# Kernel tuning notes

Hardware: AMD Instinct MI355X
Metric: run time of the kernel (lower is better)

The kernel has to match this reference:

```python
import jax, jax.numpy as jnp
import numpy as np

N = 4096
HID = 256
H = 4
D = HID // H  # 64
EDGE_DIM = 16
DEG = 32
E = N * DEG
EPS = 1e-5


def _layer_norm(x, g, b):
    m = jnp.mean(x, axis=-1, keepdims=True)
    v = jnp.mean((x - m) ** 2, axis=-1, keepdims=True)
    return (x - m) * jax.lax.rsqrt(v + EPS) * g + b


def setup_inputs() -> dict:
    key = jax.random.key(0)
    ks = jax.random.split(key, 16)
    s = 1.0 / np.sqrt(HID)
    x = jax.random.normal(ks[0], (N, HID), dtype=jnp.float32)
    # ring graph: every node is a src with DEG distinct neighbors -> no empty
    # softmax rows, no duplicate (src, dst) pairs
    src = jnp.repeat(jnp.arange(N, dtype=jnp.int64), DEG)
    dst = (src + jnp.tile(jnp.arange(1, DEG + 1, dtype=jnp.int64), N)) % N
    edge_index = jnp.stack([src, dst], axis=0)
    edge_attr = jax.random.normal(ks[1], (E, EDGE_DIM), dtype=jnp.float32)
    inp = {
        "x": x,
        "edge_index": edge_index,
        "edge_attr": edge_attr,
        "Wq": jax.random.uniform(ks[2], (HID, HID), jnp.float32, -s, s),
        "bq": jnp.zeros((HID,), jnp.float32),
        "Wk": jax.random.uniform(ks[3], (HID, HID), jnp.float32, -s, s),
        "bk": jnp.zeros((HID,), jnp.float32),
        "Wv": jax.random.uniform(ks[4], (HID, HID), jnp.float32, -s, s),
        "bv": jnp.zeros((HID,), jnp.float32),
        "Wo": jax.random.uniform(ks[5], (HID, HID), jnp.float32, -s, s),
        "bo": jnp.zeros((HID,), jnp.float32),
        "We": jax.random.uniform(ks[6], (EDGE_DIM, H), jnp.float32, -1.0 / np.sqrt(EDGE_DIM), 1.0 / np.sqrt(EDGE_DIM)),
        "be": jnp.zeros((H,), jnp.float32),
        "g1": jnp.ones((HID,), jnp.float32),
        "b1": jnp.zeros((HID,), jnp.float32),
        "g2": jnp.ones((HID,), jnp.float32),
        "b2": jnp.zeros((HID,), jnp.float32),
        "Wf1": jax.random.uniform(ks[7], (HID, 4 * HID), jnp.float32, -s, s),
        "bf1": jnp.zeros((4 * HID,), jnp.float32),
        "Wf2": jax.random.uniform(ks[8], (4 * HID, HID), jnp.float32, -1.0 / np.sqrt(4 * HID), 1.0 / np.sqrt(4 * HID)),
        "bf2": jnp.zeros((HID,), jnp.float32),
    }
    return inp


def reference(x, edge_index, edge_attr, Wq, bq, Wk, bk, Wv, bv, Wo, bo,
              We, be, g1, b1, g2, b2, Wf1, bf1, Wf2, bf2):
    src, dst = edge_index[0], edge_index[1]
    q = (x @ Wq + bq).reshape(N, H, D)
    k = (x @ Wk + bk).reshape(N, H, D)
    v = (x @ Wv + bv).reshape(N, H, D)
    edge_bias = edge_attr @ We + be                       # [E, H]
    dot = jnp.sum(q[src] * k[dst], axis=-1) / np.sqrt(D)  # [E, H]
    total_bias = dot + edge_bias                          # [E, H]
    # dense (H, N, N) logits, -inf everywhere except the E edges (as in the
    # original module)
    logits = jnp.full((H, N, N), -jnp.inf, dtype=x.dtype)
    logits = logits.at[:, src, dst].set(total_bias.T)
    attn = jax.nn.softmax(logits, axis=-1)                # [H, N, N]
    out = jnp.einsum('hnm,mhd->nhd', attn, v).reshape(N, HID)
    out = out @ Wo + bo
    x = _layer_norm(x + out, g1, b1)
    ffn = jax.nn.relu(x @ Wf1 + bf1) @ Wf2 + bf2
    x = _layer_norm(x + ffn, g2, b2)
    return x
```

## Files before the change

kernel.cpp:

```cpp
#include <hip/hip_runtime.h>
#include <cstddef>

#define N_NODES 4096
#define HIDDEN  256
#define NHEAD   4
#define DHEAD   64
#define EDGE_DIM 16
#define DEG     32
#define NEDGE   (N_NODES * DEG)
#define LN_EPS  1e-5f
#define QKV_STRIDE 768
#define KV_WIN  47

typedef short  s16x8 __attribute__((ext_vector_type(8)));
typedef float  f32x4 __attribute__((ext_vector_type(4)));
typedef unsigned short u16x8 __attribute__((ext_vector_type(8)));
typedef unsigned short u16x4 __attribute__((ext_vector_type(4)));

__device__ __forceinline__ unsigned short f2b(float f) {
    union { float f; unsigned u; } c{f};
    unsigned u = c.u;
    return (unsigned short)((u + 0x7fffu + ((u >> 16) & 1u)) >> 16);
}
__device__ __forceinline__ float b2f(unsigned short s) {
    union { unsigned u; float f; } c;
    c.u = ((unsigned)s) << 16;
    return c.f;
}
__device__ __forceinline__ int xcd_swz(int bid, int total) {
    const int q = total >> 3;
    return (bid & 7) * q + (bid >> 3);
}

__device__ __forceinline__ void pack_tile(const float* __restrict__ src,
                                          unsigned short* __restrict__ dst,
                                          int K, int Nn, int tt, int rowoff,
                                          float (*tile)[65], int tid) {
    const int tk = K / 64;
    const int k0 = (tt % tk) * 64, n0 = (tt / tk) * 64;

    const int kk = tid >> 2, nq = (tid & 3) * 16;
#pragma unroll
    for (int i = 0; i < 16; i += 4) {
        float4 vv = *(const float4*)&src[(size_t)(k0 + kk) * Nn + n0 + nq + i];
        tile[kk][nq + i + 0] = vv.x;
        tile[kk][nq + i + 1] = vv.y;
        tile[kk][nq + i + 2] = vv.z;
        tile[kk][nq + i + 3] = vv.w;
    }
    __syncthreads();
    const int nn = tid >> 2, kq = (tid & 3) * 16;
    unsigned short tmp[16];
#pragma unroll
    for (int i = 0; i < 16; ++i) tmp[i] = f2b(tile[kq + i][nn]);
    unsigned short* drow = dst + (size_t)(rowoff + n0 + nn) * K + k0 + kq;
    *(u16x8*)(drow + 0) = *(u16x8*)&tmp[0];
    *(u16x8*)(drow + 8) = *(u16x8*)&tmp[8];
}

__global__ __launch_bounds__(256) void pack_kernel(
    const float* __restrict__ Wq, const float* __restrict__ Wk,
    const float* __restrict__ Wv, const float* __restrict__ Wo,
    const float* __restrict__ Wf1, const float* __restrict__ Wf2,
    const float* __restrict__ bq, const float* __restrict__ bk,
    const float* __restrict__ bv,
    unsigned short* __restrict__ Wqkv_t, unsigned short* __restrict__ Wo_t,
    unsigned short* __restrict__ Wf1_t, unsigned short* __restrict__ Wf2_t,
    float* __restrict__ bias768) {
    const int b = blockIdx.x;
    const int tid = threadIdx.x;
    __shared__ float tile[64][65];

    if (b < 48) {
        int m = b / 16, tt = b % 16;
        const float* src = (m == 0) ? Wq : ((m == 1) ? Wk : Wv);
        pack_tile(src, Wqkv_t, 256, 256, tt, m * 256, tile, tid);
    } else if (b < 64) {
        pack_tile(Wo, Wo_t, 256, 256, b - 48, 0, tile, tid);
    } else if (b < 128) {
        pack_tile(Wf1, Wf1_t, 256, 1024, b - 64, 0, tile, tid);
    } else if (b < 192) {
        pack_tile(Wf2, Wf2_t, 1024, 256, b - 128, 0, tile, tid);
    } else {
        bias768[tid]       = bq[tid];
        bias768[256 + tid] = bk[tid];
        bias768[512 + tid] = bv[tid];
    }
}

__global__ __launch_bounds__(256) void gemm_qkv(const float* __restrict__ X,
                                                const unsigned short* __restrict__ Bt,
                                                const float* __restrict__ bias,
                                                unsigned short* __restrict__ Cout) {
    __shared__ unsigned short sA[64 * 64];
    __shared__ unsigned short sB[64 * 64];
    const int tid = threadIdx.x;
    const int wave = tid >> 6, lane = tid & 63;
    const int b2 = xcd_swz(blockIdx.x, 768);
    const int row0 = (b2 / 12) * 64, col0 = (b2 % 12) * 64;
    const int wr = wave >> 1, wc = wave & 1;

    f32x4 acc[2][2] = {};

    const int lo0 = tid * 16, lo1 = lo0 + 4096;
    const int r0 = lo0 >> 7, c0 = lo0 & 127;
    const int r1 = lo1 >> 7, c1 = lo1 & 127;
    const int so0 = (lo0 & ~127) | (c0 ^ ((r0 & 7) << 4));
    const int so1 = (lo1 & ~127) | (c1 ^ ((r1 & 7) << 4));

    const int ar  = tid >> 2;
    const int akb = (tid & 3) * 16;
    const int acb = akb * 2;
    const int axr = (ar & 7) << 4;
    const int aso0 = (ar * 128) | ((acb +  0) ^ axr);
    const int aso1 = (ar * 128) | ((acb + 16) ^ axr);

    float4 f0, f1, f2v, f3;
    s16x8 b0r, b1r;

#define QKV_LOAD(KT)                                                          \
    {                                                                         \
        const float* Ap = X + (size_t)(row0 + ar) * 256 + (KT) * 64 + akb;    \
        f0  = *(const float4*)(Ap + 0);                                       \
        f1  = *(const float4*)(Ap + 4);                                       \
        f2v = *(const float4*)(Ap + 8);                                       \
        f3  = *(const float4*)(Ap + 12);                                      \
        const char* Bb = (const char*)Bt + ((size_t)col0 * 256 + (KT) * 64) * 2; \
        b0r = *(const s16x8*)(Bb + (size_t)r0 * 512 + c0);                    \
        b1r = *(const s16x8*)(Bb + (size_t)r1 * 512 + c1);                    \
    }

    QKV_LOAD(0);
#pragma unroll
    for (int kt = 0; kt < 4; ++kt) {
        if (kt) __syncthreads();
        u16x8 pa0 = {f2b(f0.x), f2b(f0.y), f2b(f0.z), f2b(f0.w),
                     f2b(f1.x), f2b(f1.y), f2b(f1.z), f2b(f1.w)};
        u16x8 pa1 = {f2b(f2v.x), f2b(f2v.y), f2b(f2v.z), f2b(f2v.w),
                     f2b(f3.x), f2b(f3.y), f2b(f3.z), f2b(f3.w)};
        *(u16x8*)((char*)sA + aso0) = pa0;
        *(u16x8*)((char*)sA + aso1) = pa1;
        *(s16x8*)((char*)sB + so0) = b0r;
        *(s16x8*)((char*)sB + so1) = b1r;
        __syncthreads();
        if (kt < 3) QKV_LOAD(kt + 1);

        const char* sAc = (const char*)sA;
        const char* sBc = (const char*)sB;
#pragma unroll
        for (int kk = 0; kk < 64; kk += 32) {
            const int koffb = (kk + ((lane >> 4) << 3)) * 2;
            s16x8 a[2], bfr[2];
#pragma unroll
            for (int m = 0; m < 2; ++m) {
                const int r = wr * 32 + m * 16 + (lane & 15);
                int off = r * 128 + koffb;
                off ^= (r & 7) << 4;
                a[m] = *(const s16x8*)(sAc + off);
            }
#pragma unroll
            for (int n = 0; n < 2; ++n) {
                const int c = wc * 32 + n * 16 + (lane & 15);
                int off = c * 128 + koffb;
                off ^= (c & 7) << 4;
                bfr[n] = *(const s16x8*)(sBc + off);
            }
#pragma unroll
            for (int m = 0; m < 2; ++m)
#pragma unroll
                for (int n = 0; n < 2; ++n)
                    acc[m][n] = __builtin_amdgcn_mfma_f32_16x16x32_bf16(
                        a[m], bfr[n], acc[m][n], 0, 0, 0);
        }
    }
#undef QKV_LOAD

    const int crow = row0 + wr * 32 + ((lane >> 4) << 2);
    const int ccol = col0 + wc * 32 + (lane & 15);
#pragma unroll
    for (int n = 0; n < 2; ++n) {
        const int c = ccol + n * 16;
        const float bv = bias[c];
#pragma unroll
        for (int m = 0; m < 2; ++m)
#pragma unroll
            for (int j = 0; j < 4; ++j)
                Cout[(size_t)(crow + m * 16 + j) * QKV_STRIDE + c] =
                    f2b(acc[m][n][j] + bv);
    }
}

__global__ __launch_bounds__(256) void gemm_ffn1(const unsigned short* __restrict__ A,
                                                 const unsigned short* __restrict__ Bt,
                                                 const float* __restrict__ bias,
                                                 unsigned short* __restrict__ Cout) {
    constexpr int K = 256;
    __shared__ unsigned short sA[64 * 64];
    __shared__ unsigned short sB[128 * 64];
    const int tid = threadIdx.x;
    const int wave = tid >> 6, lane = tid & 63;
    const int b2 = xcd_swz(blockIdx.x, 512);
    const int row0 = (b2 >> 3) * 64, col0 = (b2 & 7) * 128;
    const int wr = wave >> 1, wc = wave & 1;

    f32x4 acc[2][4] = {};

    const int lo0 = tid * 16, lo1 = lo0 + 4096;
    const int r0 = lo0 >> 7, c0 = lo0 & 127;
    const int r1 = lo1 >> 7, c1 = lo1 & 127;
    const int so0 = (lo0 & ~127) | (c0 ^ ((r0 & 7) << 4));
    const int so1 = (lo1 & ~127) | (c1 ^ ((r1 & 7) << 4));

    s16x8 a0r, a1r, breg[4];

#define F1_LOAD(KT)                                                           \
    {                                                                         \
        const char* Ab = (const char*)A + ((size_t)row0 * K + (KT) * 64) * 2; \
        a0r = *(const s16x8*)(Ab + (size_t)r0 * (K * 2) + c0);                \
        a1r = *(const s16x8*)(Ab + (size_t)r1 * (K * 2) + c1);                \
        const char* Bb = (const char*)Bt + ((size_t)col0 * K + (KT) * 64) * 2;\
        _Pragma("unroll")                                                     \
        for (int p = 0; p < 4; ++p) {                                         \
            const int lo = tid * 16 + p * 4096;                               \
            const int r = lo >> 7, c = lo & 127;                              \
            breg[p] = *(const s16x8*)(Bb + (size_t)r * (K * 2) + c);          \
        }                                                                     \
    }

    F1_LOAD(0);
#pragma unroll
    for (int kt = 0; kt < 4; ++kt) {
        if (kt) __syncthreads();
        *(s16x8*)((char*)sA + so0) = a0r;
        *(s16x8*)((char*)sA + so1) = a1r;
#pragma unroll
        for (int p = 0; p < 4; ++p) {
            const int lo = tid * 16 + p * 4096;
            const int r = lo >> 7, c = lo & 127;
            const int so = (lo & ~127) | (c ^ ((r & 7) << 4));
            *(s16x8*)((char*)sB + so) = breg[p];
        }
        __syncthreads();
        if (kt + 1 < 4) F1_LOAD(kt + 1);

        const char* sAc = (const char*)sA;
        const char* sBc = (const char*)sB;
#pragma unroll
        for (int kk = 0; kk < 64; kk += 32) {
            const int koffb = (kk + ((lane >> 4) << 3)) * 2;
            s16x8 a[2], bfr[4];
#pragma unroll
            for (int m = 0; m < 2; ++m) {
                const int r = wr * 32 + m * 16 + (lane & 15);
                int off = r * 128 + koffb;
                off ^= (r & 7) << 4;
                a[m] = *(const s16x8*)(sAc + off);
            }
#pragma unroll
            for (int n = 0; n < 4; ++n) {
                const int c = wc * 64 + n * 16 + (lane & 15);
                int off = c * 128 + koffb;
                off ^= (c & 7) << 4;
                bfr[n] = *(const s16x8*)(sBc + off);
            }
#pragma unroll
            for (int m = 0; m < 2; ++m)
#pragma unroll
                for (int n = 0; n < 4; ++n)
                    acc[m][n] = __builtin_amdgcn_mfma_f32_16x16x32_bf16(
                        a[m], bfr[n], acc[m][n], 0, 0, 0);
        }
    }
#undef F1_LOAD

    const int crow = row0 + wr * 32 + ((lane >> 4) << 2);
    const int ccol = col0 + wc * 64 + (lane & 15);
#pragma unroll
    for (int n = 0; n < 4; ++n) {
        const int c = ccol + n * 16;
        const float bv = bias[c];
#pragma unroll
        for (int m = 0; m < 2; ++m)
#pragma unroll
            for (int j = 0; j < 4; ++j) {
                const int r = crow + m * 16 + j;
                Cout[(size_t)r * 1024 + c] = f2b(fmaxf(acc[m][n][j] + bv, 0.f));
            }
    }
}

__global__ __launch_bounds__(256) void gemm_partial(const unsigned short* __restrict__ A,
                                                    const unsigned short* __restrict__ Bt,
                                                    float* __restrict__ part) {
    constexpr int KF = 1024;
    __shared__ unsigned short sA[64 * 64];
    __shared__ unsigned short sB[64 * 64];
    const int tid = threadIdx.x;
    const int wave = tid >> 6, lane = tid & 63;
    const int b2 = xcd_swz(blockIdx.x, 512);
    const int z = b2 >> 8;
    const int rem = b2 & 255;
    const int row0 = (rem >> 2) * 64, col0 = (rem & 3) * 64;
    const int wr = wave >> 1, wc = wave & 1;

    f32x4 acc[2][2] = {};

    const int lo0 = tid * 16;
    const int lo1 = lo0 + 4096;
    const int r0 = lo0 >> 7, c0 = lo0 & 127;
    const int r1 = lo1 >> 7, c1 = lo1 & 127;
    const int so0 = (lo0 & ~127) | (c0 ^ ((r0 & 7) << 4));
    const int so1 = (lo1 & ~127) | (c1 ^ ((r1 & 7) << 4));

    const char* Abase = (const char*)A + ((size_t)row0 * KF + z * 512) * 2;
    const char* Bbase = (const char*)Bt + ((size_t)col0 * KF + z * 512) * 2;

    s16x8 a0r, a1r, b0r, b1r;

#define GP_LOAD(KT)                                                           \
    {                                                                         \
        a0r = *(const s16x8*)(Abase + (KT) * 128 + (size_t)r0 * (KF * 2) + c0); \
        a1r = *(const s16x8*)(Abase + (KT) * 128 + (size_t)r1 * (KF * 2) + c1); \
        b0r = *(const s16x8*)(Bbase + (KT) * 128 + (size_t)r0 * (KF * 2) + c0); \
        b1r = *(const s16x8*)(Bbase + (KT) * 128 + (size_t)r1 * (KF * 2) + c1); \
    }

    GP_LOAD(0);
#pragma unroll
    for (int kt = 0; kt < 8; ++kt) {
        if (kt) __syncthreads();
        *(s16x8*)((char*)sA + so0) = a0r;
        *(s16x8*)((char*)sA + so1) = a1r;
        *(s16x8*)((char*)sB + so0) = b0r;
        *(s16x8*)((char*)sB + so1) = b1r;
        __syncthreads();
        if (kt + 1 < 8) GP_LOAD(kt + 1);

        const char* sAc = (const char*)sA;
        const char* sBc = (const char*)sB;
#pragma unroll
        for (int kk = 0; kk < 64; kk += 32) {
            const int koffb = (kk + ((lane >> 4) << 3)) * 2;
            s16x8 a[2], bfr[2];
#pragma unroll
            for (int m = 0; m < 2; ++m) {
                const int r = wr * 32 + m * 16 + (lane & 15);
                int off = r * 128 + koffb;
                off ^= (r & 7) << 4;
                a[m] = *(const s16x8*)(sAc + off);
            }
#pragma unroll
            for (int n = 0; n < 2; ++n) {
                const int c = wc * 32 + n * 16 + (lane & 15);
                int off = c * 128 + koffb;
                off ^= (c & 7) << 4;
                bfr[n] = *(const s16x8*)(sBc + off);
            }
#pragma unroll
            for (int m = 0; m < 2; ++m)
#pragma unroll
                for (int n = 0; n < 2; ++n)
                    acc[m][n] = __builtin_amdgcn_mfma_f32_16x16x32_bf16(
                        a[m], bfr[n], acc[m][n], 0, 0, 0);
        }
    }
#undef GP_LOAD

    const int crow = row0 + wr * 32 + ((lane >> 4) << 2);
    const int ccol = col0 + wc * 32 + (lane & 15);
    float* pz = part + (size_t)z * N_NODES * HIDDEN;
#pragma unroll
    for (int n = 0; n < 2; ++n) {
        const int c = ccol + n * 16;
#pragma unroll
        for (int m = 0; m < 2; ++m)
#pragma unroll
            for (int j = 0; j < 4; ++j)
                pz[(size_t)(crow + m * 16 + j) * HIDDEN + c] = acc[m][n][j];
    }
}

__global__ __launch_bounds__(256) void ln2_reduce(const float* __restrict__ part,
                                                  const float* __restrict__ y,
                                                  const float* __restrict__ bf2,
                                                  const float* __restrict__ g2,
                                                  const float* __restrict__ b2,
                                                  float* __restrict__ out) {
    const int tid = threadIdx.x;
    const int row = blockIdx.x * 8 + (tid >> 5);
    const int cb = (tid & 31) * 8;
    const size_t rb = (size_t)row * HIDDEN;
    constexpr size_t ZS = (size_t)N_NODES * HIDDEN;

    float vals[8];
#pragma unroll
    for (int q = 0; q < 2; ++q) {
        const int c = cb + q * 4;
        float4 vy = *(const float4*)&y[rb + c];
        float4 vb = *(const float4*)&bf2[c];
        float4 s0 = *(const float4*)&part[0 * ZS + rb + c];
        float4 s1 = *(const float4*)&part[1 * ZS + rb + c];
        vals[q * 4 + 0] = vy.x + vb.x + s0.x + s1.x;
        vals[q * 4 + 1] = vy.y + vb.y + s0.y + s1.y;
        vals[q * 4 + 2] = vy.z + vb.z + s0.z + s1.z;
        vals[q * 4 + 3] = vy.w + vb.w + s0.w + s1.w;
    }
    float sm = 0.f, sq = 0.f;
#pragma unroll
    for (int i = 0; i < 8; ++i) { sm += vals[i]; sq = fmaf(vals[i], vals[i], sq); }
#pragma unroll
    for (int off = 16; off >= 1; off >>= 1) {
        sm += __shfl_xor(sm, off);
        sq += __shfl_xor(sq, off);
    }
    const float mean = sm * (1.f / HIDDEN);
    const float var  = sq * (1.f / HIDDEN) - mean * mean;
    const float inv  = rsqrtf(var + LN_EPS);
#pragma unroll
    for (int q = 0; q < 2; ++q) {
        const int c = cb + q * 4;
        float4 vg = *(const float4*)&g2[c];
        float4 vbb = *(const float4*)&b2[c];
        float4 o;
        o.x = (vals[q * 4 + 0] - mean) * inv * vg.x + vbb.x;
        o.y = (vals[q * 4 + 1] - mean) * inv * vg.y + vbb.y;
        o.z = (vals[q * 4 + 2] - mean) * inv * vg.z + vbb.z;
        o.w = (vals[q * 4 + 3] - mean) * inv * vg.w + vbb.w;
        *(float4*)&out[rb + c] = o;
    }
}

__global__ __launch_bounds__(512) void attn_oproj_ln(
    const unsigned short* __restrict__ qkv,
    const int* __restrict__ edge_dst,
    const float* __restrict__ edge_attr,
    const float* __restrict__ We, const float* __restrict__ be,
    const unsigned short* __restrict__ Wo_t,
    const float* __restrict__ bo,
    const float* __restrict__ x,
    const float* __restrict__ g, const float* __restrict__ b,
    float* __restrict__ y, unsigned short* __restrict__ yb) {
    __shared__ float sQ[16][260];
    __shared__ float sP[16][NHEAD][DEG];
    __shared__ int   sDst[16][DEG];
    __shared__ float sWe[EDGE_DIM * NHEAD];
    __shared__ unsigned short sKV[2][KV_WIN * 256];
    __shared__ unsigned short sA[16 * 256];
    __shared__ unsigned short sB[2][256 * 64];
    __shared__ float rs[16][8], rq[16][8];

    const int tid = threadIdx.x;
    const int wave = tid >> 6, lane = tid & 63;
    const int n0 = blockIdx.x * 16;

    {
        const int r = tid >> 5, e = (tid & 31) * 8;
        u16x8 v = *(const u16x8*)(qkv + (size_t)(n0 + r) * QKV_STRIDE + e);
#pragma unroll
        for (int i = 0; i < 8; ++i) sQ[r][e + i] = b2f(v[i]);
    }
    for (int t = tid; t < 2 * KV_WIN * 32; t += 512) {
        const int half = (t >= KV_WIN * 32) ? 1 : 0;
        const int tt = t - half * (KV_WIN * 32);
        const int rr = tt >> 5, c16 = tt & 31;
        const int gsrc = (n0 + 1 + rr) & (N_NODES - 1);
        u16x8 v = *(const u16x8*)(qkv + (size_t)gsrc * QKV_STRIDE +
                                  (half ? 512 : 256) + c16 * 8);
        const int so = rr * 512 + ((c16 ^ (rr & 7)) * 16);
        *(u16x8*)((char*)sKV[half] + so) = v;
    }
    if (tid < EDGE_DIM * NHEAD) sWe[tid] = We[tid];
    __syncthreads();

    {
        const int node = tid >> 5, j = tid & 31;
        const int dstj = edge_dst[(n0 + node) * DEG + j];
        sDst[node][j] = dstj;
        const int idx = (dstj - n0 - 1) & (N_NODES - 1);
        const char* krow = (const char*)sKV[0] + idx * 512;
        const int swz = (idx & 7);
        float lg[4];
#pragma unroll
        for (int h = 0; h < 4; ++h) {
            float dot = 0.f;
            const float* qh = &sQ[node][h * 64];
#pragma unroll
            for (int q8 = 0; q8 < 8; ++q8) {
                const int c16 = h * 8 + q8;
                u16x8 kv = *(const u16x8*)(krow + ((c16 ^ swz) * 16));
#pragma unroll
                for (int d = 0; d < 8; ++d)
                    dot = fmaf(qh[q8 * 8 + d], b2f(kv[d]), dot);
            }
            lg[h] = dot * 0.125f + be[h];
        }
        const float* ea_ = edge_attr + (size_t)((n0 + node) * DEG + j) * EDGE_DIM;
#pragma unroll
        for (int c = 0; c < EDGE_DIM; ++c) {
            const float eav = ea_[c];
#pragma unroll
            for (int h = 0; h < 4; ++h)
                lg[h] = fmaf(eav, sWe[c * NHEAD + h], lg[h]);
        }
#pragma unroll
        for (int h = 0; h < 4; ++h) {
            float mx = lg[h];
#pragma unroll
            for (int off = 16; off >= 1; off >>= 1)
                mx = fmaxf(mx, __shfl_xor(mx, off));
            float p = __expf(lg[h] - mx);
            float sum = p;
#pragma unroll
            for (int off = 16; off >= 1; off >>= 1)
                sum += __shfl_xor(sum, off);
            sP[node][h][j] = p / sum;
        }
    }
    __syncthreads();

    {
        const int node = tid >> 5, oct = tid & 31;
        const int h = oct >> 3;
        const int chunk = oct;
        float acc8[8] = {};
#pragma unroll 8
        for (int j = 0; j < DEG; ++j) {
            const float p = sP[node][h][j];
            const int idx = (sDst[node][j] - n0 - 1) & (N_NODES - 1);
            u16x8 vv = *(const u16x8*)((const char*)sKV[1] + idx * 512 +
                                       ((chunk ^ (idx & 7)) * 16));
#pragma unroll
            for (int i = 0; i < 8; ++i) acc8[i] = fmaf(p, b2f(vv[i]), acc8[i]);
        }
        u16x8 pk;
#pragma unroll
        for (int i = 0; i < 8; ++i) pk[i] = f2b(acc8[i]);
        const int so = node * 512 + ((oct * 16) ^ ((node & 7) << 4));
        *(u16x8*)((char*)sA + so) = pk;
    }

    s16x8 breg[4];
#define WO_LOAD(KT)                                                           \
    {                                                                         \
        _Pragma("unroll")                                                     \
        for (int p = 0; p < 4; ++p) {                                         \
            const int lo = tid * 16 + p * 8192;                               \
            const int r = lo >> 7, c = lo & 127;                              \
            breg[p] = *(const s16x8*)((const char*)Wo_t + (size_t)r * 512 +   \
                                      (KT) * 128 + c);                        \
        }                                                                     \
    }
#define WO_STORE(BUF)                                                         \
    {                                                                         \
        _Pragma("unroll")                                                     \
        for (int p = 0; p < 4; ++p) {                                         \
            const int lo = tid * 16 + p * 8192;                               \
            const int r = lo >> 7, c = lo & 127;                              \
            const int so = (lo & ~127) | (c ^ ((r & 7) << 4));                \
            *(s16x8*)((char*)sB[BUF] + so) = breg[p];                         \
        }                                                                     \
    }

    WO_LOAD(0);
    WO_STORE(0);
    __syncthreads();

    f32x4 acc[2] = {};
#pragma unroll
    for (int kt = 0; kt < 4; ++kt) {
        if (kt + 1 < 4) WO_LOAD(kt + 1);

        const char* sBc = (const char*)sB[kt & 1];
#pragma unroll
        for (int kk = 0; kk < 64; kk += 32) {
            const int lk = ((lane >> 4) << 3);
            s16x8 a;
            {
                const int r = lane & 15;
                const int koffb = (kt * 64 + kk + lk) * 2;
                a = *(const s16x8*)((const char*)sA + r * 512 +
                                    (koffb ^ ((r & 7) << 4)));
            }
            s16x8 bfr[2];
            const int boffb = (kk + lk) * 2;
#pragma unroll
            for (int n = 0; n < 2; ++n) {
                const int c = wave * 32 + n * 16 + (lane & 15);
                bfr[n] = *(const s16x8*)(sBc + c * 128 + (boffb ^ ((c & 7) << 4)));
            }
#pragma unroll
            for (int n = 0; n < 2; ++n)
                acc[n] = __builtin_amdgcn_mfma_f32_16x16x32_bf16(a, bfr[n], acc[n], 0, 0, 0);
        }

        if (kt + 1 < 4) {
            WO_STORE((kt + 1) & 1);
            __syncthreads();
        }
    }
#undef WO_LOAD
#undef WO_STORE

    const int rbase = ((lane >> 4) << 2);
    const int cbase = wave * 32 + (lane & 15);

    float sm[4] = {}, sq_[4] = {};
#pragma unroll
    for (int n = 0; n < 2; ++n) {
        const int c = cbase + n * 16;
        const float bv = bo[c];
#pragma unroll
        for (int j = 0; j < 4; ++j) {
            const int r = rbase + j;
            float v = acc[n][j] + bv + x[(size_t)(n0 + r) * HIDDEN + c];
            acc[n][j] = v;
            sm[j] += v;
            sq_[j] = fmaf(v, v, sq_[j]);
        }
    }
#pragma unroll
    for (int off = 8; off >= 1; off >>= 1) {
#pragma unroll
        for (int j = 0; j < 4; ++j) {
            sm[j] += __shfl_xor(sm[j], off);
            sq_[j] += __shfl_xor(sq_[j], off);
        }
    }
    if ((lane & 15) == 0) {
#pragma unroll
        for (int j = 0; j < 4; ++j) {
            rs[rbase + j][wave] = sm[j];
            rq[rbase + j][wave] = sq_[j];
        }
    }
    __syncthreads();

#pragma unroll
    for (int j = 0; j < 4; ++j) {
        const int r = rbase + j;
        float tot = 0.f, totq = 0.f;
#pragma unroll
        for (int w = 0; w < 8; ++w) { tot += rs[r][w]; totq += rq[r][w]; }
        const float mean = tot * (1.f / HIDDEN);
        const float var  = totq * (1.f / HIDDEN) - mean * mean;
        const float inv  = rsqrtf(var + LN_EPS);
#pragma unroll
        for (int n = 0; n < 2; ++n) {
            const int c = cbase + n * 16;
            const float res = (acc[n][j] - mean) * inv * g[c] + b[c];
            y[(size_t)(n0 + r) * HIDDEN + c] = res;
            yb[(size_t)(n0 + r) * HIDDEN + c] = f2b(res);
        }
    }
}

extern "C" void kernel_launch(void* const* d_in, const int* in_sizes, int n_in,
                              void* d_out, int out_size, void* d_ws, size_t ws_size,
                              hipStream_t stream) {
    const float* x   = (const float*)d_in[0];
    const int*   ei  = (const int*)d_in[1];
    const float* ea  = (const float*)d_in[2];
    const float* Wq  = (const float*)d_in[3];
    const float* bq  = (const float*)d_in[4];
    const float* Wk  = (const float*)d_in[5];
    const float* bk  = (const float*)d_in[6];
    const float* Wv  = (const float*)d_in[7];
    const float* bv  = (const float*)d_in[8];
    const float* Wo  = (const float*)d_in[9];
    const float* bo  = (const float*)d_in[10];
    const float* We  = (const float*)d_in[11];
    const float* be  = (const float*)d_in[12];
    const float* g1  = (const float*)d_in[13];
    const float* b1  = (const float*)d_in[14];
    const float* g2  = (const float*)d_in[15];
    const float* b2  = (const float*)d_in[16];
    const float* Wf1 = (const float*)d_in[17];
    const float* bf1 = (const float*)d_in[18];
    const float* Wf2 = (const float*)d_in[19];
    const float* bf2 = (const float*)d_in[20];

    char* W = (char*)d_ws;
    unsigned short* Wqkv_t  = (unsigned short*)(W + (2u << 20));
    unsigned short* Wo_t    = (unsigned short*)(W + (2u << 20) + 384 * 1024);
    unsigned short* Wf1_t   = (unsigned short*)(W + (2u << 20) + 512 * 1024);
    unsigned short* Wf2_t   = (unsigned short*)(W + (2u << 20) + 1024 * 1024);
    float*          bias768 = (float*)(W + (2u << 20) + 1536 * 1024);
    unsigned short* qkvb    = (unsigned short*)(W + (4u << 20));
    unsigned short* h1b     = (unsigned short*)(W + (4u << 20));
    float*          y       = (float*)(W + (12u << 20));
    unsigned short* yb      = (unsigned short*)(W + (16u << 20));
    float*          part    = (float*)(W + (20u << 20));

    const dim3 blk(256);

    pack_kernel<<<193, blk, 0, stream>>>(Wq, Wk, Wv, Wo, Wf1, Wf2, bq, bk, bv,
                                         Wqkv_t, Wo_t, Wf1_t, Wf2_t, bias768);

    gemm_qkv<<<768, blk, 0, stream>>>(x, Wqkv_t, bias768, qkvb);

    attn_oproj_ln<<<N_NODES / 16, dim3(512), 0, stream>>>(
        qkvb, ei + NEDGE, ea, We, be, Wo_t, bo, x, g1, b1, y, yb);

    gemm_ffn1<<<512, blk, 0, stream>>>(yb, Wf1_t, bf1, h1b);

    gemm_partial<<<512, blk, 0, stream>>>(h1b, Wf2_t, part);

    ln2_reduce<<<N_NODES / 8, blk, 0, stream>>>(part, y, bf2, g2, b2, (float*)d_out);
}
```

Baseline: 53.76 us.

## Widen QKV GEMM tiles to 64x96 and read bf16 residual in LN2

The QKV projection GEMM now uses 64x96 output tiles (512 blocks instead of 768), with each wave computing a 2x3 MFMA fragment. This gives more reuse of the A tile per block and fewer redundant fp32 reads and conversions of X. Separately, the fp32 copy of the post-LN1 activation is no longer written. The final LN reads the bf16 copy for the residual instead, cutting global traffic at the cost of residual precision.

```diff
diff --git a/kernel.cpp b/kernel.cpp
--- a/kernel.cpp
+++ b/kernel.cpp
@@ -93,20 +93,14 @@
                                                 const float* __restrict__ bias,
                                                 unsigned short* __restrict__ Cout) {
     __shared__ unsigned short sA[64 * 64];
-    __shared__ unsigned short sB[64 * 64];
+    __shared__ unsigned short sB[96 * 64];
     const int tid = threadIdx.x;
     const int wave = tid >> 6, lane = tid & 63;
-    const int b2 = xcd_swz(blockIdx.x, 768);
-    const int row0 = (b2 / 12) * 64, col0 = (b2 % 12) * 64;
+    const int b2 = xcd_swz(blockIdx.x, 512);
+    const int row0 = (b2 >> 3) * 64, col0 = (b2 & 7) * 96;
     const int wr = wave >> 1, wc = wave & 1;
 
-    f32x4 acc[2][2] = {};
-
-    const int lo0 = tid * 16, lo1 = lo0 + 4096;
-    const int r0 = lo0 >> 7, c0 = lo0 & 127;
-    const int r1 = lo1 >> 7, c1 = lo1 & 127;
-    const int so0 = (lo0 & ~127) | (c0 ^ ((r0 & 7) << 4));
-    const int so1 = (lo1 & ~127) | (c1 ^ ((r1 & 7) << 4));
+    f32x4 acc[2][3] = {};
 
     const int ar  = tid >> 2;
     const int akb = (tid & 3) * 16;
@@ -116,7 +110,7 @@
     const int aso1 = (ar * 128) | ((acb + 16) ^ axr);
 
     float4 f0, f1, f2v, f3;
-    s16x8 b0r, b1r;
+    s16x8 breg[3];
 
 #define QKV_LOAD(KT)                                                          \
     {                                                                         \
@@ -126,8 +120,12 @@
         f2v = *(const float4*)(Ap + 8);                                       \
         f3  = *(const float4*)(Ap + 12);                                      \
         const char* Bb = (const char*)Bt + ((size_t)col0 * 256 + (KT) * 64) * 2; \
-        b0r = *(const s16x8*)(Bb + (size_t)r0 * 512 + c0);                    \
-        b1r = *(const s16x8*)(Bb + (size_t)r1 * 512 + c1);                    \
+        _Pragma("unroll")                                                     \
+        for (int p = 0; p < 3; ++p) {                                         \
+            const int lo = tid * 16 + p * 4096;                               \
+            const int r = lo >> 7, c = lo & 127;                              \
+            breg[p] = *(const s16x8*)(Bb + (size_t)r * 512 + c);              \
+        }                                                                     \
     }
 
     QKV_LOAD(0);
@@ -140,8 +138,13 @@
                      f2b(f3.x), f2b(f3.y), f2b(f3.z), f2b(f3.w)};
         *(u16x8*)((char*)sA + aso0) = pa0;
         *(u16x8*)((char*)sA + aso1) = pa1;
-        *(s16x8*)((char*)sB + so0) = b0r;
-        *(s16x8*)((char*)sB + so1) = b1r;
+#pragma unroll
+        for (int p = 0; p < 3; ++p) {
+            const int lo = tid * 16 + p * 4096;
+            const int r = lo >> 7, c = lo & 127;
+            const int so = (lo & ~127) | (c ^ ((r & 7) << 4));
+            *(s16x8*)((char*)sB + so) = breg[p];
+        }
         __syncthreads();
         if (kt < 3) QKV_LOAD(kt + 1);
 
@@ -150,7 +153,7 @@
 #pragma unroll
         for (int kk = 0; kk < 64; kk += 32) {
             const int koffb = (kk + ((lane >> 4) << 3)) * 2;
-            s16x8 a[2], bfr[2];
+            s16x8 a[2], bfr[3];
 #pragma unroll
             for (int m = 0; m < 2; ++m) {
                 const int r = wr * 32 + m * 16 + (lane & 15);
@@ -159,8 +162,8 @@
                 a[m] = *(const s16x8*)(sAc + off);
             }
 #pragma unroll
-            for (int n = 0; n < 2; ++n) {
-                const int c = wc * 32 + n * 16 + (lane & 15);
+            for (int n = 0; n < 3; ++n) {
+                const int c = wc * 48 + n * 16 + (lane & 15);
                 int off = c * 128 + koffb;
                 off ^= (c & 7) << 4;
                 bfr[n] = *(const s16x8*)(sBc + off);
@@ -168,7 +171,7 @@
 #pragma unroll
             for (int m = 0; m < 2; ++m)
 #pragma unroll
-                for (int n = 0; n < 2; ++n)
+                for (int n = 0; n < 3; ++n)
                     acc[m][n] = __builtin_amdgcn_mfma_f32_16x16x32_bf16(
                         a[m], bfr[n], acc[m][n], 0, 0, 0);
         }
@@ -176,9 +179,9 @@
 #undef QKV_LOAD
 
     const int crow = row0 + wr * 32 + ((lane >> 4) << 2);
-    const int ccol = col0 + wc * 32 + (lane & 15);
-#pragma unroll
-    for (int n = 0; n < 2; ++n) {
+    const int ccol = col0 + wc * 48 + (lane & 15);
+#pragma unroll
+    for (int n = 0; n < 3; ++n) {
         const int c = ccol + n * 16;
         const float bv = bias[c];
 #pragma unroll
@@ -381,7 +384,7 @@
 }
 
 __global__ __launch_bounds__(256) void ln2_reduce(const float* __restrict__ part,
-                                                  const float* __restrict__ y,
+                                                  const unsigned short* __restrict__ yb,
                                                   const float* __restrict__ bf2,
                                                   const float* __restrict__ g2,
                                                   const float* __restrict__ b2,
@@ -392,18 +395,18 @@
     const size_t rb = (size_t)row * HIDDEN;
     constexpr size_t ZS = (size_t)N_NODES * HIDDEN;
 
+    u16x8 yv = *(const u16x8*)&yb[rb + cb];
     float vals[8];
 #pragma unroll
     for (int q = 0; q < 2; ++q) {
         const int c = cb + q * 4;
-        float4 vy = *(const float4*)&y[rb + c];
         float4 vb = *(const float4*)&bf2[c];
         float4 s0 = *(const float4*)&part[0 * ZS + rb + c];
         float4 s1 = *(const float4*)&part[1 * ZS + rb + c];
-        vals[q * 4 + 0] = vy.x + vb.x + s0.x + s1.x;
-        vals[q * 4 + 1] = vy.y + vb.y + s0.y + s1.y;
-        vals[q * 4 + 2] = vy.z + vb.z + s0.z + s1.z;
-        vals[q * 4 + 3] = vy.w + vb.w + s0.w + s1.w;
+        vals[q * 4 + 0] = b2f(yv[q * 4 + 0]) + vb.x + s0.x + s1.x;
+        vals[q * 4 + 1] = b2f(yv[q * 4 + 1]) + vb.y + s0.y + s1.y;
+        vals[q * 4 + 2] = b2f(yv[q * 4 + 2]) + vb.z + s0.z + s1.z;
+        vals[q * 4 + 3] = b2f(yv[q * 4 + 3]) + vb.w + s0.w + s1.w;
     }
     float sm = 0.f, sq = 0.f;
 #pragma unroll
@@ -439,7 +442,7 @@
     const float* __restrict__ bo,
     const float* __restrict__ x,
     const float* __restrict__ g, const float* __restrict__ b,
-    float* __restrict__ y, unsigned short* __restrict__ yb) {
+    unsigned short* __restrict__ yb) {
     __shared__ float sQ[16][260];
     __shared__ float sP[16][NHEAD][DEG];
     __shared__ int   sDst[16][DEG];
@@ -648,7 +651,6 @@
         for (int n = 0; n < 2; ++n) {
             const int c = cbase + n * 16;
             const float res = (acc[n][j] - mean) * inv * g[c] + b[c];
-            y[(size_t)(n0 + r) * HIDDEN + c] = res;
             yb[(size_t)(n0 + r) * HIDDEN + c] = f2b(res);
         }
     }
@@ -687,7 +689,6 @@
     float*          bias768 = (float*)(W + (2u << 20) + 1536 * 1024);
     unsigned short* qkvb    = (unsigned short*)(W + (4u << 20));
     unsigned short* h1b     = (unsigned short*)(W + (4u << 20));
-    float*          y       = (float*)(W + (12u << 20));
     unsigned short* yb      = (unsigned short*)(W + (16u << 20));
     float*          part    = (float*)(W + (20u << 20));
 
@@ -696,14 +697,14 @@
     pack_kernel<<<193, blk, 0, stream>>>(Wq, Wk, Wv, Wo, Wf1, Wf2, bq, bk, bv,
                                          Wqkv_t, Wo_t, Wf1_t, Wf2_t, bias768);
 
-    gemm_qkv<<<768, blk, 0, stream>>>(x, Wqkv_t, bias768, qkvb);
+    gemm_qkv<<<512, blk, 0, stream>>>(x, Wqkv_t, bias768, qkvb);
 
     attn_oproj_ln<<<N_NODES / 16, dim3(512), 0, stream>>>(
-        qkvb, ei + NEDGE, ea, We, be, Wo_t, bo, x, g1, b1, y, yb);
+        qkvb, ei + NEDGE, ea, We, be, Wo_t, bo, x, g1, b1, yb);
 
     gemm_ffn1<<<512, blk, 0, stream>>>(yb, Wf1_t, bf1, h1b);
 
     gemm_partial<<<512, blk, 0, stream>>>(h1b, Wf2_t, part);
 
-    ln2_reduce<<<N_NODES / 8, blk, 0, stream>>>(part, y, bf2, g2, b2, (float*)d_out);
-}
+    ln2_reduce<<<N_NODES / 8, blk, 0, stream>>>(part, yb, bf2, g2, b2, (float*)d_out);
+}
```

Measured after the change: 53.54 us. No clear change (-0.4%).
